# Performance work log

Hardware: AMD Instinct MI355X
Metric: run time of the kernel (lower is better)

The kernel has to match this reference:

```python
import jax, jax.numpy as jnp
import numpy as np

B, N, CIN, CV, D, H, HD, W, SHIFT = 1024, 192, 63, 27, 256, 8, 32, 8, 4
DEPTH, MLP = 2, 256  # mlp_dim = int(embed_dim * mlp_ratio) = 256


def setup_inputs() -> dict:
    key = jax.random.key(0)
    ks = iter(jax.random.split(key, 64))
    def w(*shape):
        return jax.random.normal(next(ks), shape, jnp.float32) * 0.02
    z = lambda *s: jnp.zeros(s, jnp.float32)
    o = lambda *s: jnp.ones(s, jnp.float32)
    return {
        'input_pts': jax.random.normal(next(ks), (B, N, CIN), jnp.float32),
        'input_views': jax.random.normal(next(ks), (B, CV), jnp.float32),
        'w_in': w(CIN, D), 'b_in': z(D),
        'ln_in_s': o(D), 'ln_in_b': z(D),
        'ln1_s': o(DEPTH, D), 'ln1_b': z(DEPTH, D),
        'wq': w(DEPTH, D, H, HD), 'bq': z(DEPTH, H, HD),
        'wk': w(DEPTH, D, H, HD), 'bk': z(DEPTH, H, HD),
        'wv': w(DEPTH, D, H, HD), 'bv': z(DEPTH, H, HD),
        'wo': w(DEPTH, H, HD, D), 'bo': z(DEPTH, D),
        'ln2_s': o(DEPTH, D), 'ln2_b': z(DEPTH, D),
        'w_mlp1': w(DEPTH, D, MLP), 'b_mlp1': z(DEPTH, MLP),
        'w_mlp2': w(DEPTH, MLP, D), 'b_mlp2': z(DEPTH, D),
        'w_skip': w(DEPTH, CIN + D, D), 'b_skip': z(DEPTH, D),
        'ln_f_s': o(D), 'ln_f_b': z(D),
        'w_alpha': w(D, 1), 'b_alpha': z(1),
        'w_feat': w(D, D), 'b_feat': z(D),
        'w_rgb1': w(D + CV, D // 2), 'b_rgb1': z(D // 2),
        'w_rgb2': w(D // 2, 3), 'b_rgb2': z(3),
    }


def _ln(x, s, b, eps=1e-6):
    m = jnp.mean(x, -1, keepdims=True)
    v = jnp.mean(jnp.square(x - m), -1, keepdims=True)
    return (x - m) * jax.lax.rsqrt(v + eps) * s + b


def _pos_embed(n, d):
    pos = jnp.arange(n, dtype=jnp.float32)[:, None]
    i = jnp.arange(d)
    ang = pos / jnp.power(10000.0, (2 * (i // 2)).astype(jnp.float32) / d)
    return jnp.where(i % 2 == 0, jnp.sin(ang), jnp.cos(ang))[None]  # [1, n, d]


def _block(x, shifted, ln1_s, ln1_b, wq, bq, wk, bk, wv, bv, wo, bo,
           ln2_s, ln2_b, w1, b1, w2, b2):
    b, n, c = x.shape
    y = _ln(x, ln1_s, ln1_b)
    if shifted:
        y = jnp.roll(y, -SHIFT, axis=1)
    yw = y.reshape(b * (n // W), W, c)  # window partition
    q = jnp.einsum('bnc,chd->bnhd', yw, wq) + bq
    k = jnp.einsum('bnc,chd->bnhd', yw, wk) + bk
    v = jnp.einsum('bnc,chd->bnhd', yw, wv) + bv
    scale = np.float32(1.0 / np.sqrt(HD))
    a = jax.nn.softmax(jnp.einsum('bqhd,bkhd->bhqk', q * scale, k), axis=-1)
    o = jnp.einsum('bhqk,bkhd->bqhd', a, v)
    o = jnp.einsum('bqhd,hdc->bqc', o, wo) + bo
    o = o.reshape(b, n, c)  # window reverse
    if shifted:
        o = jnp.roll(o, SHIFT, axis=1)
    x = x + o
    y = _ln(x, ln2_s, ln2_b)
    y = jax.nn.gelu(jnp.einsum('bnc,cm->bnm', y, w1) + b1)
    y = jnp.einsum('bnm,mc->bnc', y, w2) + b2
    return x + y


def reference(input_pts, input_views, w_in, b_in, ln_in_s, ln_in_b,
              ln1_s, ln1_b, wq, bq, wk, bk, wv, bv, wo, bo, ln2_s, ln2_b,
              w_mlp1, b_mlp1, w_mlp2, b_mlp2, w_skip, b_skip,
              ln_f_s, ln_f_b, w_alpha, b_alpha, w_feat, b_feat,
              w_rgb1, b_rgb1, w_rgb2, b_rgb2):
    x = input_pts @ w_in + b_in
    x = _ln(x, ln_in_s, ln_in_b)
    x = x + _pos_embed(x.shape[1], x.shape[2])
    for i in range(DEPTH):  # shift on odd layers; skips = [0, 1]
        x = _block(x, i % 2 == 1, ln1_s[i], ln1_b[i], wq[i], bq[i], wk[i], bk[i],
                   wv[i], bv[i], wo[i], bo[i], ln2_s[i], ln2_b[i],
                   w_mlp1[i], b_mlp1[i], w_mlp2[i], b_mlp2[i])
        x = jax.nn.gelu(jnp.concatenate([input_pts, x], -1) @ w_skip[i] + b_skip[i])
    h = _ln(x, ln_f_s, ln_f_b)
    alpha = h @ w_alpha + b_alpha
    feature = h @ w_feat + b_feat
    views = jnp.repeat(input_views[:, None, :], h.shape[1], axis=1)
    hr = jnp.concatenate([feature, views], -1)
    rgb = jax.nn.gelu(hr @ w_rgb1 + b_rgb1) @ w_rgb2 + b_rgb2
    return rgb, alpha
```

## Files before the change

### kernel.cpp

```cpp
#include <hip/hip_runtime.h>
#include <hip/hip_bf16.h>
#include <math.h>

typedef __hip_bfloat16 bf16;
typedef __attribute__((ext_vector_type(8))) short short8;
typedef __attribute__((ext_vector_type(4))) float f32x4;

#define T_TOK 196608
#define NSEQ  192
#define DMODEL 256
#define CHUNKS 4
#define CHUNKM (T_TOK/CHUNKS)

__device__ __forceinline__ float cvt(float v){ return v; }
__device__ __forceinline__ float cvt(bf16 v){ return __bfloat162float(v); }
__device__ __forceinline__ short bfbits(float f){
  bf16 h = __float2bfloat16(f); return *reinterpret_cast<short*>(&h);
}
__device__ __forceinline__ float bfu(unsigned short v){ return __uint_as_float(((unsigned)v) << 16); }

__device__ __forceinline__ float gelu_f(float x){
  const float k0 = 0.7978845608028654f;
  float u = k0*(x + 0.044715f*x*x*x);
  return x / (1.f + __expf(-2.f*u));
}

__device__ __forceinline__ void barrier_lgkm(){
  asm volatile("s_waitcnt lgkmcnt(0)" ::: "memory");
  __builtin_amdgcn_s_barrier();
  asm volatile("" ::: "memory");
}

__global__ __launch_bounds__(256) void pe_kernel(float* __restrict__ PE){
  int n = blockIdx.x, d = threadIdx.x;
  float e = (float)(2*(d>>1)) / 256.f;
  float ang = (float)n * powf(10000.f, -e);
  PE[n*DMODEL + d] = (d & 1) ? cosf(ang) : sinf(ang);
}

__global__ __launch_bounds__(256) void w2b_kernel(
    const float* __restrict__ src, bf16* __restrict__ dst,
    int K, int N, int KL, int dstStride, int kOff, const float* __restrict__ scale)
{
  int idx = blockIdx.x*256 + threadIdx.x;
  if (idx >= N*KL) return;
  int n = idx / KL, k = idx - n*KL;
  float v = 0.f;
  if (k < K){
    v = src[(size_t)k*N + n];
    if (scale) v *= scale[k];
  }
  dst[(size_t)n*dstStride + kOff + k] = __float2bfloat16(v);
}

__global__ __launch_bounds__(256) void ucalc_kernel(
    const float* __restrict__ W, const float* __restrict__ lnS,
    const float* __restrict__ lnB, const float* __restrict__ bias,
    float* __restrict__ u, float* __restrict__ wB, int K, int N)
{
  __shared__ float pu[4], pb[4];
  const int n = blockIdx.x;
  const int k = threadIdx.x;
  float su = 0.f, sb = 0.f;
  if (k < K){
    float w = W[(size_t)k*N + n];
    su = cvt(__float2bfloat16(lnS[k]*w));
    sb = lnB[k]*w;
  }
  #pragma unroll
  for (int off = 32; off; off >>= 1){
    su += __shfl_xor(su, off, 64);
    sb += __shfl_xor(sb, off, 64);
  }
  int lane = k & 63, wv = k >> 6;
  if (lane == 0){ pu[wv] = su; pb[wv] = sb; }
  __syncthreads();
  if (k == 0){
    u[n]  = pu[0]+pu[1]+pu[2]+pu[3];
    wB[n] = pb[0]+pb[1]+pb[2]+pb[3] + bias[n];
  }
}

__global__ __launch_bounds__(256) void pts2b_kernel(
    const float* __restrict__ src, bf16* __restrict__ dst)
{
  int idx = blockIdx.x*256 + threadIdx.x;
  int t = idx >> 6, k = idx & 63;
  dst[idx] = __float2bfloat16(k < 63 ? src[(size_t)t*63 + k] : 0.f);
}

__global__ __launch_bounds__(256) void views2b_kernel(
    const float* __restrict__ src, bf16* __restrict__ dst)
{
  int idx = blockIdx.x*256 + threadIdx.x;
  int t = idx >> 5, k = idx & 31;
  dst[idx] = __float2bfloat16(k < 27 ? src[(size_t)t*27 + k] : 0.f);
}

__global__ __launch_bounds__(256) void ln_pe_kernel(
    bf16* __restrict__ X, const float* __restrict__ s, const float* __restrict__ b,
    const float* __restrict__ PE, float* __restrict__ s1o, float* __restrict__ s2o)
{
  const int lane = threadIdx.x & 63, w = threadIdx.x >> 6;
  const size_t t = (size_t)blockIdx.x * 4 + w;
  const int n = (int)(t % NSEQ);
  const int c = lane * 4;

  ushort4 u = *reinterpret_cast<const ushort4*>(X + t*DMODEL + c);
  float x0 = bfu(u.x), x1 = bfu(u.y), x2 = bfu(u.z), x3 = bfu(u.w);

  float sx = x0 + x1 + x2 + x3;
  float sq = x0*x0 + x1*x1 + x2*x2 + x3*x3;
  #pragma unroll
  for (int off = 32; off; off >>= 1){
    sx += __shfl_xor(sx, off, 64);
    sq += __shfl_xor(sq, off, 64);
  }
  float mean = sx * (1.f/256.f);
  float var  = sq * (1.f/256.f) - mean*mean;
  float rstd = rsqrtf(var + 1e-6f);

  float4 sv = *reinterpret_cast<const float4*>(s + c);
  float4 bv = *reinterpret_cast<const float4*>(b + c);
  float4 pv = *reinterpret_cast<const float4*>(PE + n*DMODEL + c);

  float y0 = (x0 - mean)*rstd*sv.x + bv.x + pv.x;
  float y1 = (x1 - mean)*rstd*sv.y + bv.y + pv.y;
  float y2 = (x2 - mean)*rstd*sv.z + bv.z + pv.z;
  float y3 = (x3 - mean)*rstd*sv.w + bv.w + pv.w;

  ushort4 o;
  o.x = (unsigned short)bfbits(y0);
  o.y = (unsigned short)bfbits(y1);
  o.z = (unsigned short)bfbits(y2);
  o.w = (unsigned short)bfbits(y3);
  *reinterpret_cast<ushort4*>(X + t*DMODEL + c) = o;

  float sy  = y0 + y1 + y2 + y3;
  float syq = y0*y0 + y1*y1 + y2*y2 + y3*y3;
  #pragma unroll
  for (int off = 32; off; off >>= 1){
    sy  += __shfl_xor(sy,  off, 64);
    syq += __shfl_xor(syq, off, 64);
  }
  if (lane == 0){ s1o[t] = sy; s2o[t] = syq; }
}

template<int MODE, bool LNF, bool ADD, bool GELU, bool STATS>
__global__ __launch_bounds__(256) void gemm_mfma(
    const bf16* __restrict__ A1, int lda1,
    const bf16* __restrict__ A2, int lda2, int SB, int aOff,
    const float* __restrict__ s1i, const float* __restrict__ s2i,
    const float* __restrict__ uvec,
    const bf16* __restrict__ WT, int Kpad, const float* __restrict__ bias,
    bf16* __restrict__ C, int ldc, size_t segStride, int cOff, int rollShift,
    float* __restrict__ s1o, float* __restrict__ s2o)
{
  __shared__ short buf[17408];
  short* As0 = buf;
  short* As1 = buf + 5120;
  short* Cs  = buf;
  __shared__ float sScale[128], sAlpha[128];

  const int tid = threadIdx.x;
  const int lane = tid & 63, wid = tid >> 6;
  const int wm = wid >> 1, wn = wid & 1;
  const int col16 = lane & 15, quad = lane >> 4;
  const int sm = tid >> 1, half = tid & 1;
  const int m0 = blockIdx.y * 128, n0 = blockIdx.x * 128;

  f32x4 acc[4][4];
  #pragma unroll
  for (int i = 0; i < 4; i++)
    #pragma unroll
    for (int j = 0; j < 4; j++) acc[i][j] = (f32x4){0.f,0.f,0.f,0.f};

  int row = m0 + sm;
  if (MODE == 0 && rollShift){
    int bb = row / NSEQ;
    int n  = row - bb*NSEQ;
    n += rollShift; if (n >= NSEQ) n -= NSEQ;
    row = bb*NSEQ + n;
  }
  const size_t arow = (size_t)aOff + row;
  const size_t arow2 = (MODE == 3) ? (arow / NSEQ) : arow;

  if (LNF && tid < 128){
    int r2 = m0 + tid;
    if (rollShift){
      int bb = r2 / NSEQ, n = r2 - bb*NSEQ;
      n += rollShift; if (n >= NSEQ) n -= NSEQ;
      r2 = bb*NSEQ + n;
    }
    size_t r = (size_t)aOff + r2;
    float m1 = s1i[r] * (1.f/256.f);
    float m2 = s2i[r] * (1.f/256.f);
    float rs = rsqrtf(m2 - m1*m1 + 1e-6f);
    sScale[tid] = rs;
    sAlpha[tid] = -m1*rs;
  }

  auto loadA = [&](int k0, uint4& u0, uint4& u1){
    const int gk = k0 + half*16;
    const bf16* src;
    if (MODE == 0) src = A1 + arow*(size_t)lda1 + gk;
    else src = (gk < SB) ? (A1 + arow*(size_t)lda1 + gk)
                         : (A2 + arow2*(size_t)lda2 + (gk - SB));
    u0 = *(const uint4*)(src);
    u1 = *(const uint4*)(src + 8);
  };
  auto writeA = [&](short* dst, const uint4& u0, const uint4& u1){
    *(uint4*)&dst[sm*40 + half*16]     = u0;
    *(uint4*)&dst[sm*40 + half*16 + 8] = u1;
  };

  uint4 p0, p1;
  loadA(0, p0, p1);
  writeA(As0, p0, p1);
  if (Kpad > 32) loadA(32, p0, p1);
  barrier_lgkm();

  int cur = 0;
  for (int k0 = 0; k0 < Kpad; k0 += 32){
    const short* Asc = cur ? As1 : As0;
    short8 afr[4];
    #pragma unroll
    for (int mi = 0; mi < 4; mi++)
      afr[mi] = *(const short8*)&Asc[(wm*64 + mi*16 + col16)*40 + quad*8];
    short8 bfr[4];
    #pragma unroll
    for (int ni = 0; ni < 4; ni++)
      bfr[ni] = *(const short8*)((const short*)WT
                 + (size_t)(n0 + wn*64 + ni*16 + col16)*Kpad + k0 + quad*8);
    #pragma unroll
    for (int mi = 0; mi < 4; mi++)
      #pragma unroll
      for (int ni = 0; ni < 4; ni++)
        acc[mi][ni] = __builtin_amdgcn_mfma_f32_16x16x32_bf16(
            afr[mi], bfr[ni], acc[mi][ni], 0, 0, 0);
    if (k0 + 32 < Kpad){
      short* Asn = cur ? As0 : As1;
      writeA(Asn, p0, p1);
      if (k0 + 64 < Kpad) loadA(k0+64, p0, p1);
    }
    barrier_lgkm();
    cur ^= 1;
  }

  #pragma unroll
  for (int ni = 0; ni < 4; ni++){
    int ncol = wn*64 + ni*16 + col16;
    float bv = bias[n0 + ncol];
    float uv = LNF ? uvec[n0 + ncol] : 0.f;
    #pragma unroll
    for (int mi = 0; mi < 4; mi++){
      f32x4 a = acc[mi][ni];
      #pragma unroll
      for (int r = 0; r < 4; r++){
        int lrow = wm*64 + mi*16 + quad*4 + r;
        float val;
        if (LNF) val = sScale[lrow]*a[r] + sAlpha[lrow]*uv + bv;
        else     val = a[r] + bv;
        if (GELU) val = gelu_f(val);
        Cs[lrow*136 + ncol] = bfbits(val);
      }
    }
  }
  __syncthreads();

  const int seg = n0 >> 8;
  const int nb  = n0 & 255;
  const int orow = tid >> 4;
  const int ocol = (tid & 15) * 8;
  #pragma unroll
  for (int p = 0; p < 8; p++){
    int lrow = p*16 + orow;
    size_t mrow = (size_t)cOff + m0 + lrow;
    short8 v = *(const short8*)&Cs[lrow*136 + ocol];
    bf16* dst = C + (size_t)seg*segStride + mrow*ldc + nb + ocol;
    float rowSum = 0.f, rowSq = 0.f;
    if (ADD){
      short8 c = *(const short8*)dst;
      short8 o;
      #pragma unroll
      for (int e = 0; e < 8; e++){
        bf16 va, ca;
        *reinterpret_cast<short*>(&va) = v[e];
        *reinterpret_cast<short*>(&ca) = c[e];
        float f = cvt(va) + cvt(ca);
        o[e] = bfbits(f);
        if (STATS){ rowSum += f; rowSq += f*f; }
      }
      *(short8*)dst = o;
    } else {
      if (STATS){
        #pragma unroll
        for (int e = 0; e < 8; e++){
          bf16 va; *reinterpret_cast<short*>(&va) = v[e];
          float f = cvt(va);
          rowSum += f; rowSq += f*f;
        }
      }
      *(short8*)dst = v;
    }
    if (STATS){
      #pragma unroll
      for (int mk = 1; mk <= 8; mk <<= 1){
        rowSum += __shfl_xor(rowSum, mk, 64);
        rowSq  += __shfl_xor(rowSq,  mk, 64);
      }
      if ((tid & 15) == 0){
        atomicAdd(&s1o[mrow], rowSum);
        atomicAdd(&s2o[mrow], rowSq);
      }
    }
  }
}

__global__ __launch_bounds__(256) void attn_lite(
    bf16* __restrict__ Qg, const bf16* __restrict__ Kg, const bf16* __restrict__ Vg)
{
  __shared__ float qs[8][257], ks[8][257], vs[8][257];
  __shared__ float sc[8][8][8];
  const int c = threadIdx.x;
  const size_t base = (size_t)blockIdx.x * 8 * 256;
  #pragma unroll
  for (int j = 0; j < 8; j++){
    qs[j][c] = cvt(Qg[base + j*256 + c]);
    ks[j][c] = cvt(Kg[base + j*256 + c]);
    vs[j][c] = cvt(Vg[base + j*256 + c]);
  }
  __syncthreads();

  const float scale = 0.17677669529663687f;
  #pragma unroll
  for (int r = 0; r < 2; r++){
    int idx = r*256 + c;
    int h = idx >> 6, qi = (idx >> 3) & 7, ki = idx & 7;
    float s = 0.f;
    #pragma unroll
    for (int d = 0; d < 32; d++) s += qs[qi][h*32+d] * ks[ki][h*32+d];
    sc[h][qi][ki] = s * scale;
  }
  __syncthreads();

  if (c < 64){
    int h = c >> 3, qi = c & 7;
    float mx = -1e30f;
    #pragma unroll
    for (int u = 0; u < 8; u++) mx = fmaxf(mx, sc[h][qi][u]);
    float e[8], sum = 0.f;
    #pragma unroll
    for (int u = 0; u < 8; u++){ e[u] = __expf(sc[h][qi][u] - mx); sum += e[u]; }
    float inv = 1.f / sum;
    #pragma unroll
    for (int u = 0; u < 8; u++) sc[h][qi][u] = e[u] * inv;
  }
  __syncthreads();

  {
    int h = c >> 5;
    #pragma unroll
    for (int j = 0; j < 8; j++){
      float o = 0.f;
      #pragma unroll
      for (int u = 0; u < 8; u++) o += sc[h][j][u] * vs[u][c];
      Qg[base + j*256 + c] = __float2bfloat16(o);
    }
  }
}

__global__ __launch_bounds__(256) void alpha_kernel(
    const bf16* __restrict__ X, const float* __restrict__ s1,
    const float* __restrict__ s2, const float* __restrict__ s,
    const float* __restrict__ b, const float* __restrict__ wa,
    const float* __restrict__ ba, float* __restrict__ out)
{
  int lane = threadIdx.x & 63, w = threadIdx.x >> 6;
  size_t t = (size_t)blockIdx.x * 4 + w;
  float m = s1[t] * (1.f/256.f);
  float q = s2[t] * (1.f/256.f);
  float r = rsqrtf(q - m*m + 1e-6f);
  float acc = 0.f;
  #pragma unroll
  for (int j = 0; j < 4; j++){
    int c = lane + 64*j;
    float y = (cvt(X[t*DMODEL + c]) - m) * r * s[c] + b[c];
    acc += y * wa[c];
  }
  #pragma unroll
  for (int off = 32; off; off >>= 1) acc += __shfl_down(acc, off, 64);
  if (lane == 0) out[t] = acc + ba[0];
}

__global__ __launch_bounds__(256) void rgb2_kernel(
    const bf16* __restrict__ T1, const float* __restrict__ w2,
    const float* __restrict__ b2, float* __restrict__ out)
{
  int lane = threadIdx.x & 63, w = threadIdx.x >> 6;
  size_t t = (size_t)blockIdx.x * 4 + w;
  float h0 = cvt(T1[t*256 + lane]);
  float h1 = cvt(T1[t*256 + 64 + lane]);
  float a0 = h0*w2[lane*3+0] + h1*w2[(lane+64)*3+0];
  float a1 = h0*w2[lane*3+1] + h1*w2[(lane+64)*3+1];
  float a2 = h0*w2[lane*3+2] + h1*w2[(lane+64)*3+2];
  #pragma unroll
  for (int off = 32; off; off >>= 1){
    a0 += __shfl_down(a0, off, 64);
    a1 += __shfl_down(a1, off, 64);
    a2 += __shfl_down(a2, off, 64);
  }
  if (lane == 0){
    out[t*3+0] = a0 + b2[0];
    out[t*3+1] = a1 + b2[1];
    out[t*3+2] = a2 + b2[2];
  }
}

extern "C" void kernel_launch(void* const* d_in, const int* in_sizes, int n_in,
                              void* d_out, int out_size, void* d_ws, size_t ws_size,
                              hipStream_t stream)
{
  (void)in_sizes; (void)n_in; (void)out_size;
  const float* pts     = (const float*)d_in[0];
  const float* views   = (const float*)d_in[1];
  const float* w_in    = (const float*)d_in[2];
  const float* b_in    = (const float*)d_in[3];
  const float* ln_in_s = (const float*)d_in[4];
  const float* ln_in_b = (const float*)d_in[5];
  const float* ln1_s   = (const float*)d_in[6];
  const float* ln1_b   = (const float*)d_in[7];
  const float* wq      = (const float*)d_in[8];
  const float* bq      = (const float*)d_in[9];
  const float* wk      = (const float*)d_in[10];
  const float* bk      = (const float*)d_in[11];
  const float* wv      = (const float*)d_in[12];
  const float* bv      = (const float*)d_in[13];
  const float* wo      = (const float*)d_in[14];
  const float* bo      = (const float*)d_in[15];
  const float* ln2_s   = (const float*)d_in[16];
  const float* ln2_b   = (const float*)d_in[17];
  const float* w_mlp1  = (const float*)d_in[18];
  const float* b_mlp1  = (const float*)d_in[19];
  const float* w_mlp2  = (const float*)d_in[20];
  const float* b_mlp2  = (const float*)d_in[21];
  const float* w_skip  = (const float*)d_in[22];
  const float* b_skip  = (const float*)d_in[23];
  const float* ln_f_s  = (const float*)d_in[24];
  const float* ln_f_b  = (const float*)d_in[25];
  const float* w_alpha = (const float*)d_in[26];
  const float* b_alpha = (const float*)d_in[27];
  const float* w_feat  = (const float*)d_in[28];
  const float* b_feat  = (const float*)d_in[29];
  const float* w_rgb1  = (const float*)d_in[30];
  const float* b_rgb1  = (const float*)d_in[31];
  const float* w_rgb2  = (const float*)d_in[32];
  const float* b_rgb2  = (const float*)d_in[33];

  const size_t SZ = (size_t)T_TOK * DMODEL * 2;
  const size_t WT_ELEMS = 16384 + 2*(196608 + 3*65536 + 81920) + 65536 + 36864;
  const size_t UV_FLOATS = 2*768*2 + 2*256*2 + 2*256;
  const size_t NEED = 2*SZ + (size_t)4*T_TOK*4 + NSEQ*DMODEL*4 + UV_FLOATS*4
                    + WT_ELEMS*2 + (size_t)T_TOK*64*2 + 1024*32*2;
  if (ws_size < NEED) return;

  char* wsp = (char*)d_ws;
  bf16* xr = (bf16*)(wsp);
  bf16* x2 = (bf16*)(wsp + SZ);
  float* s1A = (float*)(wsp + 2*SZ);
  float* s2A = s1A + T_TOK;
  float* s1B = s2A + T_TOK;
  float* s2B = s1B + T_TOK;
  float* PE  = s2B + T_TOK;
  float* uvp = PE + NSEQ*DMODEL;
  float* uqkv[2], *wBqkv[2], *um1[2], *wBm1[2];
  {
    float* q = uvp;
    for (int i = 0; i < 2; i++){ uqkv[i] = q; q += 768; }
    for (int i = 0; i < 2; i++){ wBqkv[i] = q; q += 768; }
    for (int i = 0; i < 2; i++){ um1[i] = q; q += 256; }
    for (int i = 0; i < 2; i++){ wBm1[i] = q; q += 256; }
  }
  float* ufeat  = uvp + 2*768*2 + 2*256*2;
  float* wBfeat = ufeat + 256;
  bf16* wtp = (bf16*)(uvp + UV_FLOATS);

  bf16* wt_in = wtp;
  bf16* wt_qkv[2], *wt_o[2], *wt_m1[2], *wt_m2[2], *wt_sk[2];
  bf16* p = wt_in + 16384;
  for (int i = 0; i < 2; i++){
    wt_qkv[i] = p; p += 196608;
    wt_o[i]   = p; p += 65536;
    wt_m1[i]  = p; p += 65536;
    wt_m2[i]  = p; p += 65536;
    wt_sk[i]  = p; p += 81920;
  }
  bf16* wt_feat = p; p += 65536;
  bf16* wt_rgb1 = p; p += 36864;
  bf16* pts_b   = p; p += (size_t)T_TOK*64;
  bf16* views_b = p; p += 1024*32;

  float* out_rgb   = (float*)d_out;
  float* out_alpha = out_rgb + (size_t)T_TOK * 3;

  dim3 blk(256);
  dim3 g256(2, T_TOK/128);
  dim3 gQKV(6, CHUNKM/128);
  dim3 gC(2, CHUNKM/128);
  dim3 g128(1, T_TOK/128);
  dim3 gLN(T_TOK/4);
  dim3 gStat(T_TOK/4);
  dim3 gAttn(CHUNKM/8);

  const float* NF = nullptr;
  const bf16*  NB = nullptr;
  float* NFW = nullptr;

  pe_kernel<<<dim3(NSEQ), blk, 0, stream>>>(PE);
  pts2b_kernel<<<dim3(T_TOK*64/256), blk, 0, stream>>>(pts, pts_b);
  views2b_kernel<<<dim3(1024*32/256), blk, 0, stream>>>(views, views_b);
  #define W2B(src, dst, K_, N_, KL_, ST_, KO_, SC_) \
    w2b_kernel<<<dim3(((N_)*(KL_)+255)/256), blk, 0, stream>>>(src, dst, K_, N_, KL_, ST_, KO_, SC_)
  W2B(w_in, wt_in, 63, 256, 64, 64, 0, NF);
  for (int i = 0; i < 2; i++){
    const float* s1 = ln1_s + i*256;
    const float* b1 = ln1_b + i*256;
    W2B(wq + (size_t)i*65536, wt_qkv[i],            256, 256, 256, 256, 0, s1);
    W2B(wk + (size_t)i*65536, wt_qkv[i] + 65536,    256, 256, 256, 256, 0, s1);
    W2B(wv + (size_t)i*65536, wt_qkv[i] + 131072,   256, 256, 256, 256, 0, s1);
    ucalc_kernel<<<dim3(256), blk, 0, stream>>>(wq + (size_t)i*65536, s1, b1,
        bq + i*256, uqkv[i],       wBqkv[i],       256, 256);
    ucalc_kernel<<<dim3(256), blk, 0, stream>>>(wk + (size_t)i*65536, s1, b1,
        bk + i*256, uqkv[i] + 256, wBqkv[i] + 256, 256, 256);
    ucalc_kernel<<<dim3(256), blk, 0, stream>>>(wv + (size_t)i*65536, s1, b1,
        bv + i*256, uqkv[i] + 512, wBqkv[i] + 512, 256, 256);
    W2B(wo + (size_t)i*65536, wt_o[i],  256, 256, 256, 256, 0, NF);
    W2B(w_mlp1 + (size_t)i*65536, wt_m1[i], 256, 256, 256, 256, 0, ln2_s + i*256);
    ucalc_kernel<<<dim3(256), blk, 0, stream>>>(w_mlp1 + (size_t)i*65536,
        ln2_s + i*256, ln2_b + i*256, b_mlp1 + i*256, um1[i], wBm1[i], 256, 256);
    W2B(w_mlp2 + (size_t)i*65536, wt_m2[i], 256, 256, 256, 256, 0, NF);
    W2B(w_skip + (size_t)i*81664,            wt_sk[i], 63, 256, 64, 320, 0, NF);
    W2B(w_skip + (size_t)i*81664 + 63*256,   wt_sk[i], 256, 256, 256, 320, 64, NF);
  }
  W2B(w_feat, wt_feat, 256, 256, 256, 256, 0, ln_f_s);
  ucalc_kernel<<<dim3(256), blk, 0, stream>>>(w_feat, ln_f_s, ln_f_b, b_feat,
      ufeat, wBfeat, 256, 256);
  W2B(w_rgb1,                wt_rgb1, 256, 128, 256, 288, 0, NF);
  W2B(w_rgb1 + 256*128,      wt_rgb1, 27, 128, 32, 288, 256, NF);
  #undef W2B

  gemm_mfma<0,false,false,false,false><<<g256, blk, 0, stream>>>(pts_b, 64,
      NB, 0, 0, 0, NF, NF, NF, wt_in, 64, b_in,
      xr, 256, 0, 0, 0, NFW, NFW);
  ln_pe_kernel<<<gLN, blk, 0, stream>>>(xr, ln_in_s, ln_in_b, PE, s1A, s2A);

  for (int i = 0; i < 2; i++){
    const int shift = (i == 1) ? 4 : 0;
    const int shiftBack = (i == 1) ? (NSEQ - 4) : 0;

    hipMemsetAsync(s1B, 0, (size_t)2*T_TOK*4, stream);

    bf16* qb = x2;
    bf16* kb = x2 + (size_t)CHUNKM * 256;
    bf16* vb = x2 + (size_t)2 * CHUNKM * 256;
    for (int cch = 0; cch < CHUNKS; cch++){
      int base = cch * CHUNKM;
      gemm_mfma<0,true,false,false,false><<<gQKV, blk, 0, stream>>>(xr, 256,
          NB, 0, 0, base, s1A, s2A, uqkv[i], wt_qkv[i], 256, wBqkv[i],
          x2, 256, (size_t)CHUNKM*256, 0, shift, NFW, NFW);
      attn_lite<<<gAttn, blk, 0, stream>>>(qb, kb, vb);
      gemm_mfma<0,false,true,false,true><<<gC, blk, 0, stream>>>(qb, 256,
          NB, 0, 0, 0, NF, NF, NF, wt_o[i], 256, bo + i*256,
          xr, 256, 0, base, shiftBack, s1B, s2B);
    }

    gemm_mfma<0,true,false,true,false><<<g256, blk, 0, stream>>>(xr, 256,
        NB, 0, 0, 0, s1B, s2B, um1[i], wt_m1[i], 256, wBm1[i],
        x2, 256, 0, 0, 0, NFW, NFW);
    gemm_mfma<0,false,true,false,false><<<g256, blk, 0, stream>>>(x2, 256,
        NB, 0, 0, 0, NF, NF, NF, wt_m2[i], 256, b_mlp2 + i*256,
        xr, 256, 0, 0, 0, NFW, NFW);
    hipMemsetAsync(s1A, 0, (size_t)2*T_TOK*4, stream);
    gemm_mfma<2,false,false,true,true><<<g256, blk, 0, stream>>>(pts_b, 64,
        xr, 256, 64, 0, NF, NF, NF, wt_sk[i], 320, b_skip + i*256,
        x2, 256, 0, 0, 0, s1A, s2A);
    bf16* tmp = xr; xr = x2; x2 = tmp;
  }

  alpha_kernel<<<gStat, blk, 0, stream>>>(xr, s1A, s2A, ln_f_s, ln_f_b,
      w_alpha, b_alpha, out_alpha);
  gemm_mfma<0,true,false,false,false><<<g256, blk, 0, stream>>>(xr, 256,
      NB, 0, 0, 0, s1A, s2A, ufeat, wt_feat, 256, wBfeat,
      x2, 256, 0, 0, 0, NFW, NFW);
  gemm_mfma<3,false,false,true,false><<<g128, blk, 0, stream>>>(x2, 256,
      views_b, 32, 256, 0, NF, NF, NF, wt_rgb1, 288, b_rgb1,
      xr, 256, 0, 0, 0, NFW, NFW);
  rgb2_kernel<<<gStat, blk, 0, stream>>>(xr, w_rgb2, b_rgb2, out_rgb);
}
```

Baseline: 2.026 ms.

## Fuse MLP up and down projections into one kernel keeping hidden tile in LDS

Replaces the two MLP GEMM launches with a single kernel that computes the LN-folded first GEMM plus GELU for a 64-row tile, keeps the 64x256 hidden activations in shared memory, then runs the second GEMM and adds the residual in place. This removes the global write and re-read of the hidden activation tensor and one launch. The tradeoff is that weight fragments are read straight from global memory without LDS staging, the block tile is smaller (64 rows), and the large LDS footprint may limit occupancy.

```diff
diff --git a/kernel.cpp b/kernel.cpp
--- a/kernel.cpp
+++ b/kernel.cpp
@@ -314,6 +314,162 @@
         atomicAdd(&s2o[mrow], rowSq);
       }
     }
+  }
+}
+
+__global__ __launch_bounds__(256) void mlp_fused(
+    const bf16* __restrict__ X,
+    const float* __restrict__ s1i, const float* __restrict__ s2i,
+    const float* __restrict__ uvec,
+    const bf16* __restrict__ W1T,
+    const float* __restrict__ wB1,
+    const bf16* __restrict__ W2T,
+    const float* __restrict__ b2,
+    bf16* __restrict__ Y)
+{
+  __shared__ short sT[64*264];
+  __shared__ short buf[5120];
+  short* As0 = buf;
+  short* As1 = buf + 2560;
+  short* Cs  = sT;
+  __shared__ float sScale[64], sAlpha[64];
+
+  const int tid = threadIdx.x;
+  const int lane = tid & 63, wid = tid >> 6;
+  const int col16 = lane & 15, quad = lane >> 4;
+  const int qr = tid >> 2, qc = tid & 3;
+  const int m0 = blockIdx.x * 64;
+
+  if (tid < 64){
+    size_t r = (size_t)m0 + tid;
+    float m1 = s1i[r] * (1.f/256.f);
+    float m2 = s2i[r] * (1.f/256.f);
+    float rs = rsqrtf(m2 - m1*m1 + 1e-6f);
+    sScale[tid] = rs;
+    sAlpha[tid] = -m1*rs;
+  }
+
+  const size_t arow = (size_t)m0 + qr;
+  auto loadA = [&](int k0, uint4& u){
+    u = *(const uint4*)(X + arow*DMODEL + k0 + qc*8);
+  };
+  auto writeA = [&](short* dst, const uint4& u){
+    *(uint4*)&dst[qr*40 + qc*8] = u;
+  };
+
+  f32x4 acc[4][4];
+  #pragma unroll
+  for (int i = 0; i < 4; i++)
+    #pragma unroll
+    for (int j = 0; j < 4; j++) acc[i][j] = (f32x4){0.f,0.f,0.f,0.f};
+
+  uint4 p;
+  loadA(0, p); writeA(As0, p);
+  loadA(32, p);
+  barrier_lgkm();
+  int cur = 0;
+  for (int k0 = 0; k0 < 256; k0 += 32){
+    const short* Asc = cur ? As1 : As0;
+    short8 afr[4];
+    #pragma unroll
+    for (int mi = 0; mi < 4; mi++)
+      afr[mi] = *(const short8*)&Asc[(mi*16 + col16)*40 + quad*8];
+    short8 bfr[4];
+    #pragma unroll
+    for (int ni = 0; ni < 4; ni++)
+      bfr[ni] = *(const short8*)((const short*)W1T
+                 + (size_t)(wid*64 + ni*16 + col16)*256 + k0 + quad*8);
+    #pragma unroll
+    for (int mi = 0; mi < 4; mi++)
+      #pragma unroll
+      for (int ni = 0; ni < 4; ni++)
+        acc[mi][ni] = __builtin_amdgcn_mfma_f32_16x16x32_bf16(
+            afr[mi], bfr[ni], acc[mi][ni], 0, 0, 0);
+    if (k0 + 32 < 256){
+      short* Asn = cur ? As0 : As1;
+      writeA(Asn, p);
+      if (k0 + 64 < 256) loadA(k0 + 64, p);
+    }
+    barrier_lgkm();
+    cur ^= 1;
+  }
+
+  #pragma unroll
+  for (int ni = 0; ni < 4; ni++){
+    int ncol = wid*64 + ni*16 + col16;
+    float uv = uvec[ncol];
+    float bv = wB1[ncol];
+    #pragma unroll
+    for (int mi = 0; mi < 4; mi++){
+      f32x4 a = acc[mi][ni];
+      #pragma unroll
+      for (int r = 0; r < 4; r++){
+        int lrow = mi*16 + quad*4 + r;
+        float val = sScale[lrow]*a[r] + sAlpha[lrow]*uv + bv;
+        sT[lrow*264 + ncol] = bfbits(gelu_f(val));
+      }
+    }
+  }
+  __syncthreads();
+
+  f32x4 acc2[4][4];
+  #pragma unroll
+  for (int i = 0; i < 4; i++)
+    #pragma unroll
+    for (int j = 0; j < 4; j++) acc2[i][j] = (f32x4){0.f,0.f,0.f,0.f};
+  for (int k0 = 0; k0 < 256; k0 += 32){
+    short8 afr[4];
+    #pragma unroll
+    for (int mi = 0; mi < 4; mi++)
+      afr[mi] = *(const short8*)&sT[(mi*16 + col16)*264 + k0 + quad*8];
+    short8 bfr[4];
+    #pragma unroll
+    for (int ni = 0; ni < 4; ni++)
+      bfr[ni] = *(const short8*)((const short*)W2T
+                 + (size_t)(wid*64 + ni*16 + col16)*256 + k0 + quad*8);
+    #pragma unroll
+    for (int mi = 0; mi < 4; mi++)
+      #pragma unroll
+      for (int ni = 0; ni < 4; ni++)
+        acc2[mi][ni] = __builtin_amdgcn_mfma_f32_16x16x32_bf16(
+            afr[mi], bfr[ni], acc2[mi][ni], 0, 0, 0);
+  }
+  __syncthreads();
+
+  #pragma unroll
+  for (int ni = 0; ni < 4; ni++){
+    int ncol = wid*64 + ni*16 + col16;
+    float bv = b2[ncol];
+    #pragma unroll
+    for (int mi = 0; mi < 4; mi++){
+      f32x4 a = acc2[mi][ni];
+      #pragma unroll
+      for (int r = 0; r < 4; r++){
+        int lrow = mi*16 + quad*4 + r;
+        Cs[lrow*264 + ncol] = bfbits(a[r] + bv);
+      }
+    }
+  }
+  __syncthreads();
+
+  const int orow = tid >> 5;
+  const int oc   = (tid & 31) * 8;
+  #pragma unroll
+  for (int ppp = 0; ppp < 8; ppp++){
+    int lrow = ppp*8 + orow;
+    size_t mrow = (size_t)m0 + lrow;
+    short8 v = *(const short8*)&Cs[lrow*264 + oc];
+    bf16* dst = Y + mrow*DMODEL + oc;
+    short8 c = *(const short8*)dst;
+    short8 o;
+    #pragma unroll
+    for (int e = 0; e < 8; e++){
+      bf16 va, ca;
+      *reinterpret_cast<short*>(&va) = v[e];
+      *reinterpret_cast<short*>(&ca) = c[e];
+      o[e] = bfbits(cvt(va) + cvt(ca));
+    }
+    *(short8*)dst = o;
   }
 }
 
@@ -509,6 +665,7 @@
   dim3 gC(2, CHUNKM/128);
   dim3 g128(1, T_TOK/128);
   dim3 gLN(T_TOK/4);
+  dim3 gMLP(T_TOK/64);
   dim3 gStat(T_TOK/4);
   dim3 gAttn(CHUNKM/8);
 
@@ -574,12 +731,9 @@
           xr, 256, 0, base, shiftBack, s1B, s2B);
     }
 
-    gemm_mfma<0,true,false,true,false><<<g256, blk, 0, stream>>>(xr, 256,
-        NB, 0, 0, 0, s1B, s2B, um1[i], wt_m1[i], 256, wBm1[i],
-        x2, 256, 0, 0, 0, NFW, NFW);
-    gemm_mfma<0,false,true,false,false><<<g256, blk, 0, stream>>>(x2, 256,
-        NB, 0, 0, 0, NF, NF, NF, wt_m2[i], 256, b_mlp2 + i*256,
-        xr, 256, 0, 0, 0, NFW, NFW);
+    mlp_fused<<<gMLP, blk, 0, stream>>>(xr, s1B, s2B, um1[i],
+        wt_m1[i], wBm1[i], wt_m2[i], b_mlp2 + i*256, xr);
+
     hipMemsetAsync(s1A, 0, (size_t)2*T_TOK*4, stream);
     gemm_mfma<2,false,false,true,true><<<g256, blk, 0, stream>>>(pts_b, 64,
         xr, 256, 64, 0, NF, NF, NF, wt_sk[i], 320, b_skip + i*256,
```

Result: no change. 2.025 ms (-0.0%).
